# Optimization experiments

Measured on AMD Instinct MI355X. Metric: run time of the kernel, lower is better.

Reference implementation:

```python
import jax, jax.numpy as jnp
from jax import lax
import numpy as np

B, T, D, H, C = 256, 2048, 40, 128, 35
LN_EPS = 1e-5


def _uniform(key, shape, scale):
    return jax.random.uniform(key, shape, jnp.float32, -scale, scale)


def setup_inputs() -> dict:
    key = jax.random.key(0)
    ks = jax.random.split(key, 16)
    s = 1.0 / np.sqrt(H)  # PyTorch LSTM init scale
    inp = {
        "x": jax.random.normal(ks[0], (B, T, D), jnp.float32),
        "length": jax.random.randint(ks[1], (B,), 1, T + 1, jnp.int32),
        # layer 0 (input_size=D)
        "W_ih0": _uniform(ks[2], (4 * H, D), s),
        "W_hh0": _uniform(ks[3], (4 * H, H), s),
        "b_ih0": _uniform(ks[4], (4 * H,), s),
        "b_hh0": _uniform(ks[5], (4 * H,), s),
        # layer 1 (input_size=H)
        "W_ih1": _uniform(ks[6], (4 * H, H), s),
        "W_hh1": _uniform(ks[7], (4 * H, H), s),
        "b_ih1": _uniform(ks[8], (4 * H,), s),
        "b_hh1": _uniform(ks[9], (4 * H,), s),
        # LayerNorm + Linear head
        "ln_gamma": jnp.ones((H,), jnp.float32),
        "ln_beta": jnp.zeros((H,), jnp.float32),
        "fc_w": _uniform(ks[10], (C, H), 1.0 / np.sqrt(H)),
        "fc_b": _uniform(ks[11], (C,), 1.0 / np.sqrt(H)),
    }
    return inp


def _lstm_layer(xs, length, W_ih, W_hh, b_ih, b_hh):
    # xs: [T, B, D_in]; masked recurrence emulates pack_padded_sequence:
    # state is frozen for t >= length, so the final h equals the state at
    # each sequence's last valid step.
    Tn, Bn = xs.shape[0], xs.shape[1]
    Hn = W_hh.shape[1]
    h0 = jnp.zeros((Bn, Hn), xs.dtype)
    c0 = jnp.zeros((Bn, Hn), xs.dtype)

    def step(carry, inp):
        h, c = carry
        x_t, t = inp
        gates = x_t @ W_ih.T + b_ih + h @ W_hh.T + b_hh  # [B, 4H]
        i, f, g, o = jnp.split(gates, 4, axis=-1)  # PyTorch gate order i,f,g,o
        i = jax.nn.sigmoid(i)
        f = jax.nn.sigmoid(f)
        g = jnp.tanh(g)
        o = jax.nn.sigmoid(o)
        c_new = f * c + i * g
        h_new = o * jnp.tanh(c_new)
        m = (t < length)[:, None]
        h = jnp.where(m, h_new, h)
        c = jnp.where(m, c_new, c)
        return (h, c), h

    (h_fin, c_fin), hs = lax.scan(step, (h0, c0), (xs, jnp.arange(Tn)))
    return hs, h_fin


def reference(x, length, W_ih0, W_hh0, b_ih0, b_hh0, W_ih1, W_hh1, b_ih1, b_hh1,
              ln_gamma, ln_beta, fc_w, fc_b):
    xs = jnp.transpose(x, (1, 0, 2))  # [T, B, D]
    hs1, _ = _lstm_layer(xs, length, W_ih0, W_hh0, b_ih0, b_hh0)
    _, h_last = _lstm_layer(hs1, length, W_ih1, W_hh1, b_ih1, b_hh1)  # h[-1]: [B, H]
    # LayerNorm over feature dim
    mu = jnp.mean(h_last, axis=-1, keepdims=True)
    var = jnp.mean(jnp.square(h_last - mu), axis=-1, keepdims=True)
    hn = (h_last - mu) * lax.rsqrt(var + LN_EPS) * ln_gamma + ln_beta
    return hn @ fc_w.T + fc_b  # [B, C]
```

## Files before the change

kernel.cpp:

```cpp
#include <hip/hip_runtime.h>

#define Bn 256
#define Tn 2048
#define Dn 40
#define Hn 128
#define Cn 35

typedef _Float16 h2 __attribute__((ext_vector_type(2)));

__device__ __forceinline__ int sdot4(int a, int b, int c) {
#if __has_builtin(__builtin_amdgcn_sdot4)
  return __builtin_amdgcn_sdot4(a, b, c, false);
#else
  int r = c;
#pragma unroll
  for (int i = 0; i < 4; ++i)
    r += ((int)(a << (24 - 8 * i)) >> 24) * ((int)(b << (24 - 8 * i)) >> 24);
  return r;
#endif
}

__device__ __forceinline__ float fdot2f(h2 a, h2 b, float c) {
#if __has_builtin(__builtin_amdgcn_fdot2)
  return __builtin_amdgcn_fdot2(a, b, c, false);
#else
  return c + (float)(a[0]) * (float)(b[0]) + (float)(a[1]) * (float)(b[1]);
#endif
}

__device__ __forceinline__ h2 bch(int u) { return __builtin_bit_cast(h2, u); }

__device__ __forceinline__ int pk2i(float a, float b) {
  h2 r; r[0] = (_Float16)a; r[1] = (_Float16)b;
  return __builtin_bit_cast(int, r);
}

__device__ __forceinline__ float rcpf_(float x) {
#if __has_builtin(__builtin_amdgcn_rcpf)
  return __builtin_amdgcn_rcpf(x);
#else
  return 1.f / x;
#endif
}

__device__ __forceinline__ float sigm(float v) {
  v = fmaxf(fminf(v, 60.f), -60.f);
  return rcpf_(1.f + __expf(-v));
}

__device__ __forceinline__ float tanha(float v) {
  v = fmaxf(fminf(v, 15.f), -15.f);
  const float e = __expf(2.f * v);
  return (e - 1.f) * rcpf_(e + 1.f);
}

__device__ __forceinline__ int q8c(float v) {
  v = fminf(fmaxf(v, -127.f), 127.f);
  return (int)__builtin_rintf(v);
}

__device__ __forceinline__ int pk4(int a, int b, int c, int d) {
  return (a & 255) | ((b & 255) << 8) | ((c & 255) << 16) | (d << 24);
}

#if __has_builtin(__builtin_amdgcn_global_load_lds)
#define HAVE_GLDS 1
__device__ __forceinline__ void gl_lds16(const float* g, float* l) {
  __builtin_amdgcn_global_load_lds(
      (const __attribute__((address_space(1))) unsigned int*)(const void*)g,
      (__attribute__((address_space(3))) unsigned int*)(void*)l, 16, 0, 0);
}
#endif

__device__ __forceinline__ void quantW128(const float* __restrict__ p,
                                          int* __restrict__ q, float& sc) {
  float m = 1e-30f;
#pragma unroll
  for (int i = 0; i < 32; ++i) {
    const float4 v = reinterpret_cast<const float4*>(p)[i];
    m = fmaxf(m, fmaxf(fmaxf(fabsf(v.x), fabsf(v.y)),
                       fmaxf(fabsf(v.z), fabsf(v.w))));
  }
  const float inv = 127.f / m;
  sc = m * (1.f / 127.f);
#pragma unroll
  for (int i = 0; i < 32; ++i) {
    const float4 v = reinterpret_cast<const float4*>(p)[i];
    q[i] = pk4(q8c(v.x * inv), q8c(v.y * inv), q8c(v.z * inv), q8c(v.w * inv));
  }
}

#define RLST(w) __builtin_amdgcn_readlane(                                  \
    ((w) < 64 ? st0 : (w) < 128 ? st1 : (w) < 192 ? st2 : (w) < 256 ? st3  \
                                                        : st4), (w) & 63)

__global__ __launch_bounds__(512) void lstm2_fused(
    const float* __restrict__ x,
    const int*   __restrict__ length,
    const float* __restrict__ Wih0, const float* __restrict__ Whh0,
    const float* __restrict__ bih0, const float* __restrict__ bhh0,
    const float* __restrict__ Wih1, const float* __restrict__ Whh1,
    const float* __restrict__ bih1, const float* __restrict__ bhh1,
    const float* __restrict__ gam,  const float* __restrict__ bet,
    const float* __restrict__ fcw,  const float* __restrict__ fcb,
    float* __restrict__ out)
{
  __shared__ int   s_w0x[20][512];
  __shared__ __align__(16) float s_xraw[192 * 4];
  __shared__ int   s_xh2[2][320];
  __shared__ float s_xp[2][16][512];
  __shared__ float s_p0[4][132];
  __shared__ float s_p1[4][132];
  __shared__ int   s_hq[64];
  __shared__ float s_h1f[128];
  __shared__ float s_hn[128];

  const int tid  = threadIdx.x;
  const int lane = tid & 63;
  const int b    = blockIdx.x;
  const int len  = length[b];

  if (tid >= 256 && tid < 448) {
    const int seg0 = (tid >> 6) - 4;
    int seg = seg0 * 64 + lane;
    if (seg >= 160) seg = 0;
#if HAVE_GLDS
    gl_lds16(x + (size_t)b * Tn * Dn + seg * 4, &s_xraw[seg0 * 256]);
#else
    *(float4*)&s_xraw[seg * 4] =
        *(const float4*)(x + (size_t)b * Tn * Dn + seg * 4);
#endif
  }

  int q0h[32], q1x[32], q1h[32];
  float s0h, s1x, s1h;
  quantW128(Whh0 + (size_t)tid * Hn, q0h, s0h);
  quantW128(Wih1 + (size_t)tid * Hn, q1x, s1x);
  quantW128(Whh1 + (size_t)tid * Hn, q1h, s1h);
  s0h *= (1.f / 127.f);
  s1x *= (1.f / 127.f);
  s1h *= (1.f / 127.f);
  {
    const float* p = Wih0 + (size_t)tid * Dn;
#pragma unroll
    for (int k = 0; k < 20; ++k) s_w0x[k][tid] = pk2i(p[2 * k], p[2 * k + 1]);
  }
  const float bias0 = bih0[tid] + bhh0[tid];
  const float bias1 = bih1[tid] + bhh1[tid];

  float c0 = 0.f;
  float c1 = 0.f;

  if (tid < 64) s_hq[tid] = 0;
  __syncthreads();

  auto burst = [&](int bb) {
    const int* flat = &s_xh2[bb][0];
    const int st0 = flat[lane], st1 = flat[lane + 64], st2 = flat[lane + 128],
              st3 = flat[lane + 192], st4 = flat[lane + 256];
#pragma unroll
    for (int pass = 0; pass < 4; ++pass) {
      float a0 = 0.f, a1 = 0.f, a2 = 0.f, a3 = 0.f;
      const int r0 = pass * 4;
#pragma unroll
      for (int g = 0; g < 5; ++g) {
        const h2 w0 = bch(s_w0x[4 * g + 0][tid]);
        const h2 w1 = bch(s_w0x[4 * g + 1][tid]);
        const h2 w2 = bch(s_w0x[4 * g + 2][tid]);
        const h2 w3 = bch(s_w0x[4 * g + 3][tid]);
        a0 = fdot2f(bch(RLST(20 * (r0 + 0) + 4 * g + 0)), w0, a0);
        a0 = fdot2f(bch(RLST(20 * (r0 + 0) + 4 * g + 1)), w1, a0);
        a0 = fdot2f(bch(RLST(20 * (r0 + 0) + 4 * g + 2)), w2, a0);
        a0 = fdot2f(bch(RLST(20 * (r0 + 0) + 4 * g + 3)), w3, a0);
        a1 = fdot2f(bch(RLST(20 * (r0 + 1) + 4 * g + 0)), w0, a1);
        a1 = fdot2f(bch(RLST(20 * (r0 + 1) + 4 * g + 1)), w1, a1);
        a1 = fdot2f(bch(RLST(20 * (r0 + 1) + 4 * g + 2)), w2, a1);
        a1 = fdot2f(bch(RLST(20 * (r0 + 1) + 4 * g + 3)), w3, a1);
        a2 = fdot2f(bch(RLST(20 * (r0 + 2) + 4 * g + 0)), w0, a2);
        a2 = fdot2f(bch(RLST(20 * (r0 + 2) + 4 * g + 1)), w1, a2);
        a2 = fdot2f(bch(RLST(20 * (r0 + 2) + 4 * g + 2)), w2, a2);
        a2 = fdot2f(bch(RLST(20 * (r0 + 2) + 4 * g + 3)), w3, a2);
        a3 = fdot2f(bch(RLST(20 * (r0 + 3) + 4 * g + 0)), w0, a3);
        a3 = fdot2f(bch(RLST(20 * (r0 + 3) + 4 * g + 1)), w1, a3);
        a3 = fdot2f(bch(RLST(20 * (r0 + 3) + 4 * g + 2)), w2, a3);
        a3 = fdot2f(bch(RLST(20 * (r0 + 3) + 4 * g + 3)), w3, a3);
      }
      s_xp[bb][r0 + 0][tid] = a0;
      s_xp[bb][r0 + 1][tid] = a1;
      s_xp[bb][r0 + 2][tid] = a2;
      s_xp[bb][r0 + 3][tid] = a3;
    }
  };

  if (tid >= 256 && tid < 416) {
    const int u = tid - 256;
    const float4 v = *(const float4*)&s_xraw[4 * u];
    s_xh2[0][2 * u]     = pk2i(v.x, v.y);
    s_xh2[0][2 * u + 1] = pk2i(v.z, v.w);
  }
  __syncthreads();
  burst(0);
  __syncthreads();
  s_p0[tid >> 7][tid & 127] = bias0 + s_xp[0][0][tid];
  __syncthreads();

#pragma unroll 1
  for (int t = 0; t < len; ++t) {
    const int tl = t & 15;

    if (tid < 128) {
      const float gi = s_p0[0][tid], gf = s_p0[1][tid];
      const float gg = s_p0[2][tid], go = s_p0[3][tid];
      c0 = sigm(gf) * c0 + sigm(gi) * tanha(gg);
      const float h = sigm(go) * tanha(c0);
      ((signed char*)s_hq)[tid] = (signed char)(int)__builtin_rintf(h * 127.f);
    } else if (tid < 256) {
      if (t > 0) {
        const int u = tid - 128;
        const float gi = s_p1[0][u], gf = s_p1[1][u];
        const float gg = s_p1[2][u], go = s_p1[3][u];
        c1 = sigm(gf) * c1 + sigm(gi) * tanha(gg);
        const float h = sigm(go) * tanha(c1);
        ((signed char*)s_hq)[128 + u] =
            (signed char)(int)__builtin_rintf(h * 127.f);
      }
    } else if (tid < 416 && tl == 13) {
      const int u = tid - 256;
      const float4 v = *(const float4*)&s_xraw[4 * u];
      const int nb = ((t + 3) >> 4) & 1;
      s_xh2[nb][2 * u]     = pk2i(v.x, v.y);
      s_xh2[nb][2 * u + 1] = pk2i(v.z, v.w);
    }
    __syncthreads();

    const int vq = s_hq[lane];

    if (tid >= 256 && tid < 448 && tl == 12) {
      const int t0 = (t & ~15) + 16;
      if (t0 <= Tn - 16) {
        const int seg0 = (tid >> 6) - 4;
        int seg = seg0 * 64 + lane;
        if (seg >= 160) seg = 0;
#if HAVE_GLDS
        gl_lds16(x + ((size_t)b * Tn + t0) * Dn + seg * 4,
                 &s_xraw[seg0 * 256]);
#else
        *(float4*)&s_xraw[seg * 4] =
            *(const float4*)(x + ((size_t)b * Tn + t0) * Dn + seg * 4);
#endif
      }
    }

    const int rowi = t + 1;
    const float xacc = s_xp[(rowi >> 4) & 1][rowi & 15][tid];

    int ia = 0, ia2 = 0, ib = 0, ib2 = 0, ic = 0, ic2 = 0;
#pragma unroll
    for (int j = 0; j < 32; j += 2) {
      const int s0 = __builtin_amdgcn_readlane(vq, j);
      const int s1 = __builtin_amdgcn_readlane(vq, j + 1);
      ia  = sdot4(s0, q0h[j], ia);
      ib  = sdot4(s0, q1x[j], ib);
      ia2 = sdot4(s1, q0h[j + 1], ia2);
      ib2 = sdot4(s1, q1x[j + 1], ib2);
    }
#pragma unroll
    for (int j = 0; j < 32; j += 2) {
      const int s0 = __builtin_amdgcn_readlane(vq, 32 + j);
      const int s1 = __builtin_amdgcn_readlane(vq, 33 + j);
      ic  = sdot4(s0, q1h[j], ic);
      ic2 = sdot4(s1, q1h[j + 1], ic2);
    }
    s_p0[tid >> 7][tid & 127] = bias0 + xacc + (float)(ia + ia2) * s0h;
    s_p1[tid >> 7][tid & 127] =
        bias1 + (float)(ib + ib2) * s1x + (float)(ic + ic2) * s1h;

    if (tl == 14) burst(((t + 2) >> 4) & 1);
    __syncthreads();
  }

  if (tid >= 128 && tid < 256) {
    const int u = tid - 128;
    const float gi = s_p1[0][u], gf = s_p1[1][u];
    const float gg = s_p1[2][u], go = s_p1[3][u];
    c1 = sigm(gf) * c1 + sigm(gi) * tanha(gg);
    s_h1f[u] = sigm(go) * tanha(c1);
  }
  __syncthreads();

  if (tid < 64) {
    const float a = s_h1f[tid], d = s_h1f[64 + tid];
    float s = a + d, q = a * a + d * d;
#pragma unroll
    for (int m = 32; m >= 1; m >>= 1) {
      s += __shfl_xor(s, m, 64);
      q += __shfl_xor(q, m, 64);
    }
    const float mu = s * (1.f / 128.f);
    float var = q * (1.f / 128.f) - mu * mu;
    var = fmaxf(var, 0.f);
    const float rstd = rsqrtf(var + 1e-5f);
    s_hn[tid]      = (a - mu) * rstd * gam[tid]      + bet[tid];
    s_hn[64 + tid] = (d - mu) * rstd * gam[64 + tid] + bet[64 + tid];
  }
  __syncthreads();

  if (tid < Cn) {
    float acc = fcb[tid];
    const float* wp = fcw + tid * Hn;
#pragma unroll 4
    for (int k = 0; k < Hn; ++k) acc += s_hn[k] * wp[k];
    out[(size_t)b * Cn + tid] = acc;
  }
}

extern "C" void kernel_launch(void* const* d_in, const int* in_sizes, int n_in,
                              void* d_out, int out_size, void* d_ws, size_t ws_size,
                              hipStream_t stream) {
  (void)in_sizes; (void)n_in; (void)d_ws; (void)ws_size; (void)out_size;
  lstm2_fused<<<dim3(Bn), dim3(512), 0, stream>>>(
      (const float*)d_in[0],  (const int*)d_in[1],
      (const float*)d_in[2],  (const float*)d_in[3],
      (const float*)d_in[4],  (const float*)d_in[5],
      (const float*)d_in[6],  (const float*)d_in[7],
      (const float*)d_in[8],  (const float*)d_in[9],
      (const float*)d_in[10], (const float*)d_in[11],
      (const float*)d_in[12], (const float*)d_in[13],
      (float*)d_out);
}
```

Measured before the change: 2.510 ms.

## Remap gate rows so cell updates use cross-lane permutes, one barrier per step

Threads are remapped so the four gates (i,f,g,o) of each hidden unit sit in adjacent lanes of one wavefront. Each thread gathers its unit's gates with ds_bpermute and updates the cell state redundantly, instead of writing gates to shared memory and reading them back after a second barrier. The hidden-state buffer is double-buffered, so each timestep needs only one __syncthreads. The cost is that every thread now evaluates the transcendental cell updates for both layers, and the loop runs one extra iteration to finish layer 1.

```diff
diff --git a/kernel.cpp b/kernel.cpp
--- a/kernel.cpp
+++ b/kernel.cpp
@@ -61,6 +61,11 @@
 
 __device__ __forceinline__ int pk4(int a, int b, int c, int d) {
   return (a & 255) | ((b & 255) << 8) | ((c & 255) << 16) | (d << 24);
+}
+
+__device__ __forceinline__ float bperm_f(int byte_idx, float v) {
+  return __builtin_bit_cast(
+      float, __builtin_amdgcn_ds_bpermute(byte_idx, __builtin_bit_cast(int, v)));
 }
 
 #if __has_builtin(__builtin_amdgcn_global_load_lds)
@@ -109,14 +114,16 @@
   __shared__ __align__(16) float s_xraw[192 * 4];
   __shared__ int   s_xh2[2][320];
   __shared__ float s_xp[2][16][512];
-  __shared__ float s_p0[4][132];
-  __shared__ float s_p1[4][132];
-  __shared__ int   s_hq[64];
+  __shared__ int   s_hq[2][64];
   __shared__ float s_h1f[128];
   __shared__ float s_hn[128];
 
   const int tid  = threadIdx.x;
   const int lane = tid & 63;
+  const int wav  = tid >> 6;
+  const int g    = lane & 3;
+  const int u    = 16 * wav + (lane >> 2);
+  const int row  = 128 * g + u;
   const int b    = blockIdx.x;
   const int len  = length[b];
 
@@ -134,24 +141,24 @@
 
   int q0h[32], q1x[32], q1h[32];
   float s0h, s1x, s1h;
-  quantW128(Whh0 + (size_t)tid * Hn, q0h, s0h);
-  quantW128(Wih1 + (size_t)tid * Hn, q1x, s1x);
-  quantW128(Whh1 + (size_t)tid * Hn, q1h, s1h);
+  quantW128(Whh0 + (size_t)row * Hn, q0h, s0h);
+  quantW128(Wih1 + (size_t)row * Hn, q1x, s1x);
+  quantW128(Whh1 + (size_t)row * Hn, q1h, s1h);
   s0h *= (1.f / 127.f);
   s1x *= (1.f / 127.f);
   s1h *= (1.f / 127.f);
   {
-    const float* p = Wih0 + (size_t)tid * Dn;
+    const float* p = Wih0 + (size_t)row * Dn;
 #pragma unroll
     for (int k = 0; k < 20; ++k) s_w0x[k][tid] = pk2i(p[2 * k], p[2 * k + 1]);
   }
-  const float bias0 = bih0[tid] + bhh0[tid];
-  const float bias1 = bih1[tid] + bhh1[tid];
+  const float bias0 = bih0[row] + bhh0[row];
+  const float bias1 = bih1[row] + bhh1[row];
 
   float c0 = 0.f;
   float c1 = 0.f;
 
-  if (tid < 64) s_hq[tid] = 0;
+  if (tid < 128) ((int*)s_hq)[tid] = 0;
   __syncthreads();
 
   auto burst = [&](int bb) {
@@ -163,27 +170,27 @@
       float a0 = 0.f, a1 = 0.f, a2 = 0.f, a3 = 0.f;
       const int r0 = pass * 4;
 #pragma unroll
-      for (int g = 0; g < 5; ++g) {
-        const h2 w0 = bch(s_w0x[4 * g + 0][tid]);
-        const h2 w1 = bch(s_w0x[4 * g + 1][tid]);
-        const h2 w2 = bch(s_w0x[4 * g + 2][tid]);
-        const h2 w3 = bch(s_w0x[4 * g + 3][tid]);
-        a0 = fdot2f(bch(RLST(20 * (r0 + 0) + 4 * g + 0)), w0, a0);
-        a0 = fdot2f(bch(RLST(20 * (r0 + 0) + 4 * g + 1)), w1, a0);
-        a0 = fdot2f(bch(RLST(20 * (r0 + 0) + 4 * g + 2)), w2, a0);
-        a0 = fdot2f(bch(RLST(20 * (r0 + 0) + 4 * g + 3)), w3, a0);
-        a1 = fdot2f(bch(RLST(20 * (r0 + 1) + 4 * g + 0)), w0, a1);
-        a1 = fdot2f(bch(RLST(20 * (r0 + 1) + 4 * g + 1)), w1, a1);
-        a1 = fdot2f(bch(RLST(20 * (r0 + 1) + 4 * g + 2)), w2, a1);
-        a1 = fdot2f(bch(RLST(20 * (r0 + 1) + 4 * g + 3)), w3, a1);
-        a2 = fdot2f(bch(RLST(20 * (r0 + 2) + 4 * g + 0)), w0, a2);
-        a2 = fdot2f(bch(RLST(20 * (r0 + 2) + 4 * g + 1)), w1, a2);
-        a2 = fdot2f(bch(RLST(20 * (r0 + 2) + 4 * g + 2)), w2, a2);
-        a2 = fdot2f(bch(RLST(20 * (r0 + 2) + 4 * g + 3)), w3, a2);
-        a3 = fdot2f(bch(RLST(20 * (r0 + 3) + 4 * g + 0)), w0, a3);
-        a3 = fdot2f(bch(RLST(20 * (r0 + 3) + 4 * g + 1)), w1, a3);
-        a3 = fdot2f(bch(RLST(20 * (r0 + 3) + 4 * g + 2)), w2, a3);
-        a3 = fdot2f(bch(RLST(20 * (r0 + 3) + 4 * g + 3)), w3, a3);
+      for (int gg = 0; gg < 5; ++gg) {
+        const h2 w0 = bch(s_w0x[4 * gg + 0][tid]);
+        const h2 w1 = bch(s_w0x[4 * gg + 1][tid]);
+        const h2 w2 = bch(s_w0x[4 * gg + 2][tid]);
+        const h2 w3 = bch(s_w0x[4 * gg + 3][tid]);
+        a0 = fdot2f(bch(RLST(20 * (r0 + 0) + 4 * gg + 0)), w0, a0);
+        a0 = fdot2f(bch(RLST(20 * (r0 + 0) + 4 * gg + 1)), w1, a0);
+        a0 = fdot2f(bch(RLST(20 * (r0 + 0) + 4 * gg + 2)), w2, a0);
+        a0 = fdot2f(bch(RLST(20 * (r0 + 0) + 4 * gg + 3)), w3, a0);
+        a1 = fdot2f(bch(RLST(20 * (r0 + 1) + 4 * gg + 0)), w0, a1);
+        a1 = fdot2f(bch(RLST(20 * (r0 + 1) + 4 * gg + 1)), w1, a1);
+        a1 = fdot2f(bch(RLST(20 * (r0 + 1) + 4 * gg + 2)), w2, a1);
+        a1 = fdot2f(bch(RLST(20 * (r0 + 1) + 4 * gg + 3)), w3, a1);
+        a2 = fdot2f(bch(RLST(20 * (r0 + 2) + 4 * gg + 0)), w0, a2);
+        a2 = fdot2f(bch(RLST(20 * (r0 + 2) + 4 * gg + 1)), w1, a2);
+        a2 = fdot2f(bch(RLST(20 * (r0 + 2) + 4 * gg + 2)), w2, a2);
+        a2 = fdot2f(bch(RLST(20 * (r0 + 2) + 4 * gg + 3)), w3, a2);
+        a3 = fdot2f(bch(RLST(20 * (r0 + 3) + 4 * gg + 0)), w0, a3);
+        a3 = fdot2f(bch(RLST(20 * (r0 + 3) + 4 * gg + 1)), w1, a3);
+        a3 = fdot2f(bch(RLST(20 * (r0 + 3) + 4 * gg + 2)), w2, a3);
+        a3 = fdot2f(bch(RLST(20 * (r0 + 3) + 4 * gg + 3)), w3, a3);
       }
       s_xp[bb][r0 + 0][tid] = a0;
       s_xp[bb][r0 + 1][tid] = a1;
@@ -193,47 +200,22 @@
   };
 
   if (tid >= 256 && tid < 416) {
-    const int u = tid - 256;
-    const float4 v = *(const float4*)&s_xraw[4 * u];
-    s_xh2[0][2 * u]     = pk2i(v.x, v.y);
-    s_xh2[0][2 * u + 1] = pk2i(v.z, v.w);
+    const int uu = tid - 256;
+    const float4 v = *(const float4*)&s_xraw[4 * uu];
+    s_xh2[0][2 * uu]     = pk2i(v.x, v.y);
+    s_xh2[0][2 * uu + 1] = pk2i(v.z, v.w);
   }
   __syncthreads();
   burst(0);
   __syncthreads();
-  s_p0[tid >> 7][tid & 127] = bias0 + s_xp[0][0][tid];
-  __syncthreads();
+
+  const int pb = (lane & ~3) << 2;
 
 #pragma unroll 1
-  for (int t = 0; t < len; ++t) {
+  for (int t = 0; t <= len; ++t) {
     const int tl = t & 15;
 
-    if (tid < 128) {
-      const float gi = s_p0[0][tid], gf = s_p0[1][tid];
-      const float gg = s_p0[2][tid], go = s_p0[3][tid];
-      c0 = sigm(gf) * c0 + sigm(gi) * tanha(gg);
-      const float h = sigm(go) * tanha(c0);
-      ((signed char*)s_hq)[tid] = (signed char)(int)__builtin_rintf(h * 127.f);
-    } else if (tid < 256) {
-      if (t > 0) {
-        const int u = tid - 128;
-        const float gi = s_p1[0][u], gf = s_p1[1][u];
-        const float gg = s_p1[2][u], go = s_p1[3][u];
-        c1 = sigm(gf) * c1 + sigm(gi) * tanha(gg);
-        const float h = sigm(go) * tanha(c1);
-        ((signed char*)s_hq)[128 + u] =
-            (signed char)(int)__builtin_rintf(h * 127.f);
-      }
-    } else if (tid < 416 && tl == 13) {
-      const int u = tid - 256;
-      const float4 v = *(const float4*)&s_xraw[4 * u];
-      const int nb = ((t + 3) >> 4) & 1;
-      s_xh2[nb][2 * u]     = pk2i(v.x, v.y);
-      s_xh2[nb][2 * u + 1] = pk2i(v.z, v.w);
-    }
-    __syncthreads();
-
-    const int vq = s_hq[lane];
+    const int vq = s_hq[t & 1][lane];
 
     if (tid >= 256 && tid < 448 && tl == 12) {
       const int t0 = (t & ~15) + 16;
@@ -249,10 +231,15 @@
             *(const float4*)(x + ((size_t)b * Tn + t0) * Dn + seg * 4);
 #endif
       }
-    }
-
-    const int rowi = t + 1;
-    const float xacc = s_xp[(rowi >> 4) & 1][rowi & 15][tid];
+    } else if (tid >= 256 && tid < 416 && tl == 13) {
+      const int uu = tid - 256;
+      const float4 v = *(const float4*)&s_xraw[4 * uu];
+      const int nb = ((t + 3) >> 4) & 1;
+      s_xh2[nb][2 * uu]     = pk2i(v.x, v.y);
+      s_xh2[nb][2 * uu + 1] = pk2i(v.z, v.w);
+    }
+
+    const float xacc = s_xp[(t >> 4) & 1][tl][tid];
 
     int ia = 0, ia2 = 0, ib = 0, ib2 = 0, ic = 0, ic2 = 0;
 #pragma unroll
@@ -271,22 +258,37 @@
       ic  = sdot4(s0, q1h[j], ic);
       ic2 = sdot4(s1, q1h[j + 1], ic2);
     }
-    s_p0[tid >> 7][tid & 127] = bias0 + xacc + (float)(ia + ia2) * s0h;
-    s_p1[tid >> 7][tid & 127] =
-        bias1 + (float)(ib + ib2) * s1x + (float)(ic + ic2) * s1h;
+    const float g0v = bias0 + xacc + (float)(ia + ia2) * s0h;
+    const float g1v = bias1 + (float)(ib + ib2) * s1x + (float)(ic + ic2) * s1h;
+
+    const float Ai = bperm_f(pb,      g0v);
+    const float Af = bperm_f(pb + 4,  g0v);
+    const float Ag = bperm_f(pb + 8,  g0v);
+    const float Ao = bperm_f(pb + 12, g0v);
+    const float Bi = bperm_f(pb,      g1v);
+    const float Bf = bperm_f(pb + 4,  g1v);
+    const float Bg = bperm_f(pb + 8,  g1v);
+    const float Bo = bperm_f(pb + 12, g1v);
+
+    if (t < len) {
+      c0 = sigm(Af) * c0 + sigm(Ai) * tanha(Ag);
+      const float h0 = sigm(Ao) * tanha(c0);
+      if (g == 0)
+        ((signed char*)&s_hq[(t + 1) & 1][0])[u] =
+            (signed char)(int)__builtin_rintf(h0 * 127.f);
+    }
+    if (t > 0) {
+      c1 = sigm(Bf) * c1 + sigm(Bi) * tanha(Bg);
+      const float h1 = sigm(Bo) * tanha(c1);
+      if (g == 1)
+        ((signed char*)&s_hq[(t + 1) & 1][0])[128 + u] =
+            (signed char)(int)__builtin_rintf(h1 * 127.f);
+      if (g == 2 && t == len) s_h1f[u] = h1;
+    }
 
     if (tl == 14) burst(((t + 2) >> 4) & 1);
     __syncthreads();
   }
-
-  if (tid >= 128 && tid < 256) {
-    const int u = tid - 128;
-    const float gi = s_p1[0][u], gf = s_p1[1][u];
-    const float gg = s_p1[2][u], go = s_p1[3][u];
-    c1 = sigm(gf) * c1 + sigm(gi) * tanha(gg);
-    s_h1f[u] = sigm(go) * tanha(c1);
-  }
-  __syncthreads();
 
   if (tid < 64) {
     const float a = s_h1f[tid], d = s_h1f[64 + tid];
```

New measurement: 3.388 ms. 34.9% more time.
